# Kernel tuning notes

Measured on AMD Instinct MI355X. Metric: run time of the kernel, lower is better.

## Reference

```python
import jax, jax.numpy as jnp
import numpy as np

EPS = 1e-8
N = 1024          # number of points
C = 16            # channels per layer
RBF_LOW, RBF_HIGH, RBF_COUNT = 0.0, 3.5, 32


def _rand(key, shape, scale=0.1):
    return scale * jax.random.normal(key, shape, dtype=jnp.float32)


def setup_inputs() -> dict:
    key = jax.random.key(0)
    ks = jax.random.split(key, 20)
    R = RBF_COUNT
    return {
        'points':   jax.random.normal(ks[0], (N, 3), dtype=jnp.float32),
        # layer 1: 2 radial filters (0->0 and 0->1), output_dim = 1 input channel
        'l1_W1':    _rand(ks[1],  (2, R, R)),
        'l1_B1':    _rand(ks[2],  (2, R)),
        'l1_W2':    _rand(ks[3],  (2, R, 1)),
        'l1_B2':    _rand(ks[4],  (2, 1)),
        'l1_si0_w': _rand(ks[5],  (C, 1)),
        'l1_si0_b': _rand(ks[6],  (C,)),
        'l1_si1_w': _rand(ks[7],  (C, 1)),
        'l1_nl_b':  _rand(ks[8],  (C,)),
        # layer 2: 5 radial filters (0->0, 0->1, 1->0, 1->1 id, 1->1 levi-civita)
        'l2_W1':    _rand(ks[9],  (5, R, R)),
        'l2_B1':    _rand(ks[10], (5, R)),
        'l2_W2':    _rand(ks[11], (5, R, C)),
        'l2_B2':    _rand(ks[12], (5, C)),
        'l2_si0_w': _rand(ks[13], (C, 2 * C)),
        'l2_si0_b': _rand(ks[14], (C,)),
        'l2_si1_w': _rand(ks[15], (C, 3 * C)),
        'l2_nl_b':  _rand(ks[16], (C,)),
        # readout
        'fc_w':     _rand(ks[17], (C, 8)),
        'fc_b':     _rand(ks[18], (8,)),
    }


def _eijk():
    e = np.zeros((3, 3, 3), dtype=np.float32)
    e[0, 1, 2] = e[1, 2, 0] = e[2, 0, 1] = 1.0
    e[0, 2, 1] = e[2, 1, 0] = e[1, 0, 2] = -1.0
    return jnp.asarray(e)


def _norm_eps(x, axis, keepdims=False):
    # norm_with_epsilon: sqrt(max(sum(x^2), EPS))
    return jnp.sqrt(jnp.maximum(jnp.sum(x * x, axis=axis, keepdims=keepdims), EPS))


def _radial(rbf, w1, b1, w2, b2):
    # R(): two-layer relu MLP on rbf features -> [N, N, F]
    h = jax.nn.relu(rbf @ w1 + b1)
    return h @ w2 + b2


def _geometry(points):
    rij = points[:, None, :] - points[None, :, :]          # [N,N,3]
    ss = jnp.sum(rij * rij, axis=-1)                        # [N,N]
    mask0 = ss < EPS                                        # dij == 0 (diagonal)
    dij = jnp.where(mask0, 0.0, jnp.sqrt(jnp.where(mask0, 1.0, ss)))
    centers = jnp.linspace(RBF_LOW, RBF_HIGH, RBF_COUNT, dtype=jnp.float32)
    gamma = jnp.float32(RBF_COUNT / (RBF_HIGH - RBF_LOW))
    rbf = jnp.exp(-gamma * (dij[..., None] - centers) ** 2)  # [N,N,RBF]
    unit = rij / _norm_eps(rij, axis=-1, keepdims=True)       # unit_vectors
    return rbf, unit, mask0


def _F1(rad, unit, mask0):
    # F_1: mask radial where dij==0, multiply by unit vectors -> [N,N,F,3]
    mr = jnp.where(mask0[..., None], 0.0, rad)
    return mr[..., None] * unit[:, :, None, :]


def _nonlinearity(x0, x1, b1):
    # degree-0: pointwise elu; degree-1: norm nonlinearity x * elu(|x|+b)/|x|
    x0 = jax.nn.elu(x0)
    n = _norm_eps(x1, axis=-1)                              # [N,C]
    x1 = x1 * (jax.nn.elu(n + b1) / n)[..., None]
    return x0, x1


def reference(points, l1_W1, l1_B1, l1_W2, l1_B2, l1_si0_w, l1_si0_b, l1_si1_w,
              l1_nl_b, l2_W1, l2_B1, l2_W2, l2_B2, l2_si0_w, l2_si0_b, l2_si1_w,
              l2_nl_b, fc_w, fc_b):
    rbf, unit, mask0 = _geometry(points)
    eijk = _eijk().astype(points.dtype)
    n_pts = points.shape[0]
    x0 = jnp.ones((n_pts, 1, 1), dtype=points.dtype)        # degree-0 input [N,1,1]

    # ---- layer 1: only degree-0 input -> (0->0) and (0->1) filters ----
    r00 = _radial(rbf, l1_W1[0], l1_B1[0], l1_W2[0], l1_B2[0])
    out0 = jnp.einsum('abf,bfi->afi', r00, x0)              # filter_0
    F1a = _F1(_radial(rbf, l1_W1[1], l1_B1[1], l1_W2[1], l1_B2[1]), unit, mask0)
    out1 = jnp.einsum('abfi,bf->afi', F1a, x0[..., 0])
    x0 = jnp.einsum('afi,gf->agi', out0, l1_si0_w) + l1_si0_b[:, None]
    x1 = jnp.einsum('afi,gf->agi', out1, l1_si1_w)
    x0, x1 = _nonlinearity(x0, x1, l1_nl_b)                 # [N,C,1], [N,C,3]

    # ---- layer 2: degree-0 and degree-1 inputs -> 5 filters ----
    rads = [_radial(rbf, l2_W1[i], l2_B1[i], l2_W2[i], l2_B2[i]) for i in range(5)]
    c00 = jnp.einsum('abf,bfi->afi', rads[0], x0)                          # 0x0->0
    c01 = jnp.einsum('abfi,bf->afi', _F1(rads[1], unit, mask0), x0[..., 0])  # 0x1->1
    c10 = jnp.einsum('abfj,bfj->af', _F1(rads[2], unit, mask0), x1)[..., None]  # 1x1->0
    c11 = jnp.einsum('abf,bfi->afi', rads[3], x1)                          # 1x0->1
    c11x = jnp.einsum('ijk,abfj,bfk->afi', eijk, _F1(rads[4], unit, mask0), x1)  # 1x1->1
    cat0 = jnp.concatenate([c00, c10], axis=-2)             # [N,2C,1]
    cat1 = jnp.concatenate([c01, c11, c11x], axis=-2)       # [N,3C,3]
    x0 = jnp.einsum('afi,gf->agi', cat0, l2_si0_w) + l2_si0_b[:, None]
    x1 = jnp.einsum('afi,gf->agi', cat1, l2_si1_w)
    x0, x1 = _nonlinearity(x0, x1, l2_nl_b)

    # ---- readout: invariant degree-0 features, mean-pool over points ----
    g = jnp.mean(x0[..., 0], axis=0)                        # [C]
    return g @ fc_w + fc_b                                  # [num_classes]
```

## Files before the change

### kernel.cpp

```cpp
#include <hip/hip_runtime.h>
#include <hip/hip_bf16.h>
#include <math.h>

#define NP 1024
#define R 32
#define C 16
#define GAMMA (32.0f/3.5f)
#define DC (3.5f/31.0f)
#define NBANK 32

typedef __attribute__((ext_vector_type(8))) short bf16x8;
typedef __attribute__((ext_vector_type(4))) float f32x4;

__device__ __forceinline__ short tobf(float x){
    __hip_bfloat16 h = __float2bfloat16(x);
    return __builtin_bit_cast(short, h);
}
__device__ __forceinline__ unsigned pack2bf(float a, float b){
    const unsigned lo = (unsigned short)tobf(a);
    const unsigned hi = (unsigned short)tobf(b);
    return lo | (hi << 16);
}
__device__ __forceinline__ float eluf(float x){ return x > 0.f ? x : expm1f(x); }

__device__ __forceinline__ f32x4 mfma16(bf16x8 a, bf16x8 b, f32x4 c){
    return __builtin_amdgcn_mfma_f32_16x16x32_bf16(a, b, c, 0, 0, 0);
}

template<int STRIDE>
__device__ __forceinline__ void load_bfrag(const float* __restrict__ src, int q, int n,
                                           bf16x8& w){
    #pragma unroll
    for (int jj = 0; jj < 8; jj++)
        w[jj] = tobf(src[(q*8+jj)*STRIDE + n]);
}

__global__ __launch_bounds__(256) void k_l1p(
    const float* __restrict__ points,
    const float* __restrict__ W1, const float* __restrict__ B1,
    const float* __restrict__ W2, const float* __restrict__ B2,
    const float* __restrict__ si0w, const float* __restrict__ si0b,
    const float* __restrict__ si1w, const float* __restrict__ nlb,
    float* __restrict__ x0g, float* __restrict__ x1s,
    float* __restrict__ c00g, float* __restrict__ c10g,
    unsigned* __restrict__ cntA,
    float* __restrict__ partial, unsigned* __restrict__ cnt)
{
    __shared__ float sS0[4][32];
    __shared__ float sT[4][32][3];
    __shared__ float sUp[4][3];
    __shared__ float sO[4];

    const int tid  = threadIdx.x;
    const int lane = tid & 63;
    const int wv   = tid >> 6;
    const int l16  = lane & 15;
    const int q    = lane >> 4;
    const int a    = blockIdx.x;
    const float pax = points[a*3+0], pay = points[a*3+1], paz = points[a*3+2];

    bf16x8 w1f[2][2];
    float  b1v[2][2];
    #pragma unroll
    for (int fi = 0; fi < 2; fi++)
        #pragma unroll
        for (int nt = 0; nt < 2; nt++){
            load_bfrag<R>(W1 + fi*R*R, q, nt*16 + l16, w1f[fi][nt]);
            b1v[fi][nt] = B1[fi*R + nt*16 + l16];
        }

    float s0a[2] = {0.f, 0.f};
    float T[2][3] = {};
    float upx = 0.f, upy = 0.f, upz = 0.f;

    for (int bt = 0; bt < 16; bt++){
        const int bA = bt*64 + wv*16 + l16;
        const float rx = pax - points[bA*3+0];
        const float ry = pay - points[bA*3+1];
        const float rz = paz - points[bA*3+2];
        const float ss = rx*rx + ry*ry + rz*rz;
        const float dij = sqrtf(ss);
        const float inv = 1.0f / sqrtf(fmaxf(ss, 1e-8f));
        const float ux = rx*inv, uy = ry*inv, uz = rz*inv;
        upx += ux; upy += uy; upz += uz;

        bf16x8 afrag;
        #pragma unroll
        for (int jj = 0; jj < 8; jj++){
            const float t = dij - (float)(q*8+jj)*DC;
            afrag[jj] = tobf(__expf(-GAMMA*t*t));
        }

        float uxr[4], uyr[4], uzr[4];
        #pragma unroll
        for (int r4 = 0; r4 < 4; r4++){
            const int sl = q*4 + r4;
            uxr[r4] = __shfl(ux, sl, 16);
            uyr[r4] = __shfl(uy, sl, 16);
            uzr[r4] = __shfl(uz, sl, 16);
        }

        #pragma unroll
        for (int nt = 0; nt < 2; nt++){
            f32x4 c = {b1v[0][nt], b1v[0][nt], b1v[0][nt], b1v[0][nt]};
            c = mfma16(afrag, w1f[0][nt], c);
            s0a[nt] += fmaxf(c[0],0.f)+fmaxf(c[1],0.f)+fmaxf(c[2],0.f)+fmaxf(c[3],0.f);
        }
        #pragma unroll
        for (int nt = 0; nt < 2; nt++){
            f32x4 c = {b1v[1][nt], b1v[1][nt], b1v[1][nt], b1v[1][nt]};
            c = mfma16(afrag, w1f[1][nt], c);
            #pragma unroll
            for (int r4 = 0; r4 < 4; r4++){
                const float h = fmaxf(c[r4], 0.f);
                T[nt][0] = fmaf(h, uxr[r4], T[nt][0]);
                T[nt][1] = fmaf(h, uyr[r4], T[nt][1]);
                T[nt][2] = fmaf(h, uzr[r4], T[nt][2]);
            }
        }
    }

    #pragma unroll
    for (int nt = 0; nt < 2; nt++){
        s0a[nt] += __shfl_down(s0a[nt], 32, 64);
        s0a[nt] += __shfl_down(s0a[nt], 16, 64);
        #pragma unroll
        for (int i = 0; i < 3; i++){
            T[nt][i] += __shfl_down(T[nt][i], 32, 64);
            T[nt][i] += __shfl_down(T[nt][i], 16, 64);
        }
    }
    #pragma unroll
    for (int off = 32; off > 0; off >>= 1){
        upx += __shfl_down(upx, off, 64);
        upy += __shfl_down(upy, off, 64);
        upz += __shfl_down(upz, off, 64);
    }
    if (lane < 16){
        sS0[wv][lane]      = s0a[0];
        sS0[wv][16 + lane] = s0a[1];
        #pragma unroll
        for (int i = 0; i < 3; i++){
            sT[wv][lane][i]      = T[0][i];
            sT[wv][16 + lane][i] = T[1][i];
        }
    }
    if (lane == 0){ sUp[wv][0] = upx; sUp[wv][1] = upy; sUp[wv][2] = upz; }
    __syncthreads();
    if (tid == 0){
        float o0 = 0.f;
        for (int j = 0; j < R; j++){
            const float S = sS0[0][j] + sS0[1][j] + sS0[2][j] + sS0[3][j];
            o0 = fmaf(S, W2[j], o0);
        }
        sO[0] = o0 + (float)NP * B2[0];
        for (int i = 0; i < 3; i++){
            float t = 0.f;
            for (int j = 0; j < R; j++){
                const float Tj = sT[0][j][i] + sT[1][j][i] + sT[2][j][i] + sT[3][j][i];
                t = fmaf(Tj, W2[R + j], t);
            }
            const float Ui = 0.25f * (sUp[0][i] + sUp[1][i] + sUp[2][i] + sUp[3][i]);
            sO[1+i] = t + B2[1] * Ui;
        }
    }
    __syncthreads();
    if (tid < C){
        const int g = tid;
        const float o0 = sO[0];
        const float o1x = sO[1], o1y = sO[2], o1z = sO[3];
        x0g[a*C+g] = eluf(fmaf(o0, si0w[g], si0b[g]));
        const float w = si1w[g];
        const float tx = o1x*w, ty = o1y*w, tz = o1z*w;
        const float n = sqrtf(fmaxf(tx*tx + ty*ty + tz*tz, 1e-8f));
        const float sc = eluf(n + nlb[g]) / n;
        x1s[0*NP*C + a*C+g] = tx*sc;
        x1s[1*NP*C + a*C+g] = ty*sc;
        x1s[2*NP*C + a*C+g] = tz*sc;
    }
    if (tid < C){ c00g[a*C + tid] = 0.f; c10g[a*C + tid] = 0.f; }
    if (tid == 0) cntA[a] = 0u;
    if (a == 0){
        partial[tid]       = 0.f;
        partial[256 + tid] = 0.f;
        if (tid < NBANK) cnt[tid] = 0u;
        if (tid == 0) cnt[NBANK] = 0u;
    }
}

__global__ __launch_bounds__(256) void k_l2r(
    const float* __restrict__ points,
    const float* __restrict__ W1, const float* __restrict__ B1,
    const float* __restrict__ W2, const float* __restrict__ B2,
    const float* __restrict__ x0g, const float* __restrict__ x1s,
    const float* __restrict__ si0w, const float* __restrict__ si0b,
    const float* __restrict__ fcw, const float* __restrict__ fcb,
    float* __restrict__ c00g, float* __restrict__ c10g,
    unsigned* __restrict__ cntA,
    float* __restrict__ partial, unsigned* __restrict__ cnt,
    float* __restrict__ out)
{
    __shared__ __align__(16) short sH[4][2][16*40];
    __shared__ float sRed[4][2][16];
    __shared__ float sP[16];
    __shared__ unsigned aDone, amLast;

    const int tid  = threadIdx.x;
    const int lane = tid & 63;
    const int wv   = tid >> 6;
    const int l16  = lane & 15;
    const int q    = lane >> 4;
    const int a    = blockIdx.x >> 1;
    const int half = blockIdx.x & 1;
    const float pax = points[a*3+0], pay = points[a*3+1], paz = points[a*3+2];

    bf16x8 w1f[2][2], w2f[2];
    float  b1v[2][2], b2v[2];
    #pragma unroll
    for (int fi = 0; fi < 2; fi++){
        const int fx = (fi == 0) ? 0 : 2;
        #pragma unroll
        for (int nt = 0; nt < 2; nt++){
            load_bfrag<R>(W1 + fx*R*R, q, 2*l16 + nt, w1f[fi][nt]);
            b1v[fi][nt] = B1[fx*R + 2*l16 + nt];
        }
        load_bfrag<C>(W2 + fx*R*C, q, l16, w2f[fi]);
        b2v[fi] = B2[fx*C + l16];
    }

    float acc0 = 0.f, acc1 = 0.f;
    short* sH0 = sH[wv][0];
    short* sH1 = sH[wv][1];

    for (int bt = half*8; bt < half*8 + 8; bt++){
        const int bA = bt*64 + wv*16 + l16;
        const float rx = pax - points[bA*3+0];
        const float ry = pay - points[bA*3+1];
        const float rz = paz - points[bA*3+2];
        const float ss = rx*rx + ry*ry + rz*rz;
        const float dij = sqrtf(ss);
        const float inv = 1.0f / sqrtf(fmaxf(ss, 1e-8f));
        const float ux = rx*inv, uy = ry*inv, uz = rz*inv;

        float uxr[4], uyr[4], uzr[4];
        #pragma unroll
        for (int r4 = 0; r4 < 4; r4++){
            const int sl = q*4 + r4;
            uxr[r4] = __shfl(ux, sl, 16);
            uyr[r4] = __shfl(uy, sl, 16);
            uzr[r4] = __shfl(uz, sl, 16);
        }

        const int rb = (bt*64 + wv*16 + q*4)*C + l16;
        float x0v[4], udv[4];
        #pragma unroll
        for (int r4 = 0; r4 < 4; r4++){
            x0v[r4] = x0g[rb + r4*C];
            const float v0 = x1s[0*NP*C + rb + r4*C];
            const float v1 = x1s[1*NP*C + rb + r4*C];
            const float v2 = x1s[2*NP*C + rb + r4*C];
            udv[r4] = uxr[r4]*v0 + uyr[r4]*v1 + uzr[r4]*v2;
        }

        bf16x8 afrag;
        #pragma unroll
        for (int jj = 0; jj < 8; jj++){
            const float t = dij - (float)(q*8+jj)*DC;
            afrag[jj] = tobf(__expf(-GAMMA*t*t));
        }

        #pragma unroll
        for (int fi = 0; fi < 2; fi++){
            f32x4 c0 = {b1v[fi][0], b1v[fi][0], b1v[fi][0], b1v[fi][0]};
            c0 = mfma16(afrag, w1f[fi][0], c0);
            f32x4 c1 = {b1v[fi][1], b1v[fi][1], b1v[fi][1], b1v[fi][1]};
            c1 = mfma16(afrag, w1f[fi][1], c1);
            short* sHf = (fi == 0) ? sH0 : sH1;
            #pragma unroll
            for (int r4 = 0; r4 < 4; r4++){
                const unsigned p = pack2bf(fmaxf(c0[r4], 0.f), fmaxf(c1[r4], 0.f));
                *(unsigned*)&sHf[(q*4+r4)*40 + 2*l16] = p;
            }
        }
        asm volatile("s_waitcnt lgkmcnt(0)" ::: "memory");

        {
            const bf16x8 hf = *(const bf16x8*)(sH0 + l16*40 + q*8);
            f32x4 d = {0.f, 0.f, 0.f, 0.f};
            d = mfma16(hf, w2f[0], d);
            #pragma unroll
            for (int r4 = 0; r4 < 4; r4++)
                acc0 = fmaf(d[r4] + b2v[0], x0v[r4], acc0);
        }
        {
            const bf16x8 hf = *(const bf16x8*)(sH1 + l16*40 + q*8);
            f32x4 d = {0.f, 0.f, 0.f, 0.f};
            d = mfma16(hf, w2f[1], d);
            #pragma unroll
            for (int r4 = 0; r4 < 4; r4++)
                acc1 = fmaf(d[r4] + b2v[1], udv[r4], acc1);
        }
    }

    acc0 += __shfl_down(acc0, 32, 64); acc0 += __shfl_down(acc0, 16, 64);
    acc1 += __shfl_down(acc1, 32, 64); acc1 += __shfl_down(acc1, 16, 64);
    if (lane < 16){ sRed[wv][0][lane] = acc0; sRed[wv][1][lane] = acc1; }
    __syncthreads();
    if (tid < 16)
        atomicAdd(&c00g[a*C + tid],
                  sRed[0][0][tid] + sRed[1][0][tid] + sRed[2][0][tid] + sRed[3][0][tid]);
    else if (tid < 32){
        const int f = tid - 16;
        atomicAdd(&c10g[a*C + f],
                  sRed[0][1][f] + sRed[1][1][f] + sRed[2][1][f] + sRed[3][1][f]);
    }
    __syncthreads();
    if (tid == 0)
        aDone = (atomicAdd(&cntA[a], 1u) == 1u) ? 1u : 0u;
    __syncthreads();

    if (aDone){
        if (tid < C){
            const int g = tid;
            float s = si0b[g];
            #pragma unroll
            for (int f = 0; f < C; f++){
                const float v0 = __hip_atomic_load(&c00g[a*C + f], __ATOMIC_RELAXED,
                                                   __HIP_MEMORY_SCOPE_AGENT);
                s = fmaf(v0, si0w[g*2*C + f], s);
            }
            #pragma unroll
            for (int f = 0; f < C; f++){
                const float v1 = __hip_atomic_load(&c10g[a*C + f], __ATOMIC_RELAXED,
                                                   __HIP_MEMORY_SCOPE_AGENT);
                s = fmaf(v1, si0w[g*2*C + C + f], s);
            }
            atomicAdd(&partial[(a & (NBANK-1))*C + g], eluf(s));
        }
        __syncthreads();
        if (tid == 0){
            amLast = 0u;
            const unsigned p1 = atomicAdd(&cnt[a & (NBANK-1)], 1u);
            if (p1 == (NP/NBANK) - 1u){
                const unsigned p2 = atomicAdd(&cnt[NBANK], 1u);
                if (p2 == NBANK - 1u) amLast = 1u;
            }
        }
        __syncthreads();
        if (amLast){
            if (tid < C){
                float v = 0.f;
                #pragma unroll
                for (int b = 0; b < NBANK; b++)
                    v += __hip_atomic_load(&partial[b*C + tid], __ATOMIC_RELAXED,
                                           __HIP_MEMORY_SCOPE_AGENT);
                sP[tid] = v;
            }
            __syncthreads();
            if (tid < 8){
                float s = fcb[tid];
                #pragma unroll
                for (int g = 0; g < C; g++)
                    s = fmaf(sP[g] * (1.0f / (float)NP), fcw[g*8 + tid], s);
                out[tid] = s;
            }
        }
    }
}

extern "C" void kernel_launch(void* const* d_in, const int* in_sizes, int n_in,
                              void* d_out, int out_size, void* d_ws, size_t ws_size,
                              hipStream_t stream)
{
    (void)in_sizes; (void)n_in; (void)out_size; (void)ws_size;
    const float* points   = (const float*)d_in[0];
    const float* l1_W1    = (const float*)d_in[1];
    const float* l1_B1    = (const float*)d_in[2];
    const float* l1_W2    = (const float*)d_in[3];
    const float* l1_B2    = (const float*)d_in[4];
    const float* l1_si0_w = (const float*)d_in[5];
    const float* l1_si0_b = (const float*)d_in[6];
    const float* l1_si1_w = (const float*)d_in[7];
    const float* l1_nl_b  = (const float*)d_in[8];
    const float* l2_W1    = (const float*)d_in[9];
    const float* l2_B1    = (const float*)d_in[10];
    const float* l2_W2    = (const float*)d_in[11];
    const float* l2_B2    = (const float*)d_in[12];
    const float* l2_si0_w = (const float*)d_in[13];
    const float* l2_si0_b = (const float*)d_in[14];
    const float* fc_w     = (const float*)d_in[17];
    const float* fc_b     = (const float*)d_in[18];

    float* ws       = (float*)d_ws;
    float* x0g      = ws;
    float* x1s      = x0g + NP*C;
    float* c00g     = x1s + 3*NP*C;
    float* c10g     = c00g + NP*C;
    float* partial  = c10g + NP*C;
    unsigned* cnt   = (unsigned*)(partial + NBANK*C);
    unsigned* cntA  = cnt + NBANK + 1;

    k_l1p<<<NP, 256, 0, stream>>>(points, l1_W1, l1_B1, l1_W2, l1_B2,
                                  l1_si0_w, l1_si0_b, l1_si1_w, l1_nl_b,
                                  x0g, x1s, c00g, c10g, cntA, partial, cnt);
    k_l2r<<<2*NP, 256, 0, stream>>>(points, l2_W1, l2_B1, l2_W2, l2_B2,
                                    x0g, x1s, l2_si0_w, l2_si0_b,
                                    fc_w, fc_b, c00g, c10g, cntA,
                                    partial, cnt, (float*)d_out);
}
```

Baseline: 155.8 us.

## Split layer-1 pass across two blocks per point with atomic merge and interleaved layout

Layer 1 now launches two blocks per point, each handling half of the neighbour tiles. W2 is applied before the reduction so only seven scalars per wave are reduced and atomically accumulated. The last-arriving block applies the nonlinearity and writes x0 and x1 interleaved as one float4 per channel, so layer 2 can load them with a single vector read. Workspace zeroing moves to a memset, which adds an extra launch plus atomic and counter overhead in exchange for more parallelism in layer 1.

```diff
diff --git a/kernel.cpp b/kernel.cpp
--- a/kernel.cpp
+++ b/kernel.cpp
@@ -41,26 +41,24 @@
     const float* __restrict__ W2, const float* __restrict__ B2,
     const float* __restrict__ si0w, const float* __restrict__ si0b,
     const float* __restrict__ si1w, const float* __restrict__ nlb,
-    float* __restrict__ x0g, float* __restrict__ x1s,
-    float* __restrict__ c00g, float* __restrict__ c10g,
-    unsigned* __restrict__ cntA,
-    float* __restrict__ partial, unsigned* __restrict__ cnt)
+    float* __restrict__ xall, float* __restrict__ l1c,
+    unsigned* __restrict__ cntL1)
 {
-    __shared__ float sS0[4][32];
-    __shared__ float sT[4][32][3];
-    __shared__ float sUp[4][3];
-    __shared__ float sO[4];
+    __shared__ float sW[4][8];
+    __shared__ float sFin[8];
+    __shared__ unsigned sAm;
 
     const int tid  = threadIdx.x;
     const int lane = tid & 63;
     const int wv   = tid >> 6;
     const int l16  = lane & 15;
     const int q    = lane >> 4;
-    const int a    = blockIdx.x;
+    const int a    = blockIdx.x >> 1;
+    const int half = blockIdx.x & 1;
     const float pax = points[a*3+0], pay = points[a*3+1], paz = points[a*3+2];
 
     bf16x8 w1f[2][2];
-    float  b1v[2][2];
+    float  b1v[2][2], w2s[2], w2t[2];
     #pragma unroll
     for (int fi = 0; fi < 2; fi++)
         #pragma unroll
@@ -68,12 +66,17 @@
             load_bfrag<R>(W1 + fi*R*R, q, nt*16 + l16, w1f[fi][nt]);
             b1v[fi][nt] = B1[fi*R + nt*16 + l16];
         }
+    #pragma unroll
+    for (int nt = 0; nt < 2; nt++){
+        w2s[nt] = W2[nt*16 + l16];
+        w2t[nt] = W2[R + nt*16 + l16];
+    }
 
     float s0a[2] = {0.f, 0.f};
     float T[2][3] = {};
     float upx = 0.f, upy = 0.f, upz = 0.f;
 
-    for (int bt = 0; bt < 16; bt++){
+    for (int bt = half*8; bt < half*8 + 8; bt++){
         const int bA = bt*64 + wv*16 + l16;
         const float rx = pax - points[bA*3+0];
         const float ry = pay - points[bA*3+1];
@@ -120,71 +123,46 @@
         }
     }
 
-    #pragma unroll
-    for (int nt = 0; nt < 2; nt++){
-        s0a[nt] += __shfl_down(s0a[nt], 32, 64);
-        s0a[nt] += __shfl_down(s0a[nt], 16, 64);
-        #pragma unroll
-        for (int i = 0; i < 3; i++){
-            T[nt][i] += __shfl_down(T[nt][i], 32, 64);
-            T[nt][i] += __shfl_down(T[nt][i], 16, 64);
-        }
-    }
-    #pragma unroll
-    for (int off = 32; off > 0; off >>= 1){
-        upx += __shfl_down(upx, off, 64);
-        upy += __shfl_down(upy, off, 64);
-        upz += __shfl_down(upz, off, 64);
-    }
-    if (lane < 16){
-        sS0[wv][lane]      = s0a[0];
-        sS0[wv][16 + lane] = s0a[1];
-        #pragma unroll
-        for (int i = 0; i < 3; i++){
-            sT[wv][lane][i]      = T[0][i];
-            sT[wv][16 + lane][i] = T[1][i];
-        }
-    }
-    if (lane == 0){ sUp[wv][0] = upx; sUp[wv][1] = upy; sUp[wv][2] = upz; }
-    __syncthreads();
-    if (tid == 0){
-        float o0 = 0.f;
-        for (int j = 0; j < R; j++){
-            const float S = sS0[0][j] + sS0[1][j] + sS0[2][j] + sS0[3][j];
-            o0 = fmaf(S, W2[j], o0);
-        }
-        sO[0] = o0 + (float)NP * B2[0];
-        for (int i = 0; i < 3; i++){
-            float t = 0.f;
-            for (int j = 0; j < R; j++){
-                const float Tj = sT[0][j][i] + sT[1][j][i] + sT[2][j][i] + sT[3][j][i];
-                t = fmaf(Tj, W2[R + j], t);
-            }
-            const float Ui = 0.25f * (sUp[0][i] + sUp[1][i] + sUp[2][i] + sUp[3][i]);
-            sO[1+i] = t + B2[1] * Ui;
-        }
-    }
-    __syncthreads();
-    if (tid < C){
-        const int g = tid;
-        const float o0 = sO[0];
-        const float o1x = sO[1], o1y = sO[2], o1z = sO[3];
-        x0g[a*C+g] = eluf(fmaf(o0, si0w[g], si0b[g]));
-        const float w = si1w[g];
-        const float tx = o1x*w, ty = o1y*w, tz = o1z*w;
-        const float n = sqrtf(fmaxf(tx*tx + ty*ty + tz*tz, 1e-8f));
-        const float sc = eluf(n + nlb[g]) / n;
-        x1s[0*NP*C + a*C+g] = tx*sc;
-        x1s[1*NP*C + a*C+g] = ty*sc;
-        x1s[2*NP*C + a*C+g] = tz*sc;
-    }
-    if (tid < C){ c00g[a*C + tid] = 0.f; c10g[a*C + tid] = 0.f; }
-    if (tid == 0) cntA[a] = 0u;
-    if (a == 0){
-        partial[tid]       = 0.f;
-        partial[256 + tid] = 0.f;
-        if (tid < NBANK) cnt[tid] = 0u;
-        if (tid == 0) cnt[NBANK] = 0u;
+    float v[7];
+    v[0] = s0a[0]*w2s[0] + s0a[1]*w2s[1];
+    #pragma unroll
+    for (int i = 0; i < 3; i++)
+        v[1+i] = T[0][i]*w2t[0] + T[1][i]*w2t[1];
+    v[4] = upx; v[5] = upy; v[6] = upz;
+    #pragma unroll
+    for (int off = 32; off > 0; off >>= 1)
+        #pragma unroll
+        for (int k = 0; k < 7; k++)
+            v[k] += __shfl_down(v[k], off, 64);
+    if (lane == 0)
+        #pragma unroll
+        for (int k = 0; k < 7; k++) sW[wv][k] = v[k];
+    __syncthreads();
+    if (tid < 7)
+        atomicAdd(&l1c[a*8 + tid], sW[0][tid] + sW[1][tid] + sW[2][tid] + sW[3][tid]);
+    __syncthreads();
+    if (tid == 0)
+        sAm = (atomicAdd(&cntL1[a], 1u) == 1u) ? 1u : 0u;
+    __syncthreads();
+    if (sAm){
+        if (tid < 7)
+            sFin[tid] = __hip_atomic_load(&l1c[a*8 + tid], __ATOMIC_RELAXED,
+                                          __HIP_MEMORY_SCOPE_AGENT);
+        __syncthreads();
+        if (tid < C){
+            const int g = tid;
+            const float o0  = sFin[0] + (float)NP * B2[0];
+            const float o1x = sFin[1] + B2[1] * 0.25f * sFin[4];
+            const float o1y = sFin[2] + B2[1] * 0.25f * sFin[5];
+            const float o1z = sFin[3] + B2[1] * 0.25f * sFin[6];
+            const float x0 = eluf(fmaf(o0, si0w[g], si0b[g]));
+            const float w = si1w[g];
+            const float tx = o1x*w, ty = o1y*w, tz = o1z*w;
+            const float n = sqrtf(fmaxf(tx*tx + ty*ty + tz*tz, 1e-8f));
+            const float sc = eluf(n + nlb[g]) / n;
+            f32x4 st = {x0, tx*sc, ty*sc, tz*sc};
+            *(f32x4*)&xall[(a*C + g)*4] = st;
+        }
     }
 }
 
@@ -192,7 +170,7 @@
     const float* __restrict__ points,
     const float* __restrict__ W1, const float* __restrict__ B1,
     const float* __restrict__ W2, const float* __restrict__ B2,
-    const float* __restrict__ x0g, const float* __restrict__ x1s,
+    const float* __restrict__ xall,
     const float* __restrict__ si0w, const float* __restrict__ si0b,
     const float* __restrict__ fcw, const float* __restrict__ fcb,
     float* __restrict__ c00g, float* __restrict__ c10g,
@@ -251,15 +229,13 @@
             uzr[r4] = __shfl(uz, sl, 16);
         }
 
-        const int rb = (bt*64 + wv*16 + q*4)*C + l16;
+        const f32x4* xp = (const f32x4*)&xall[((bt*64 + wv*16 + q*4)*C + l16)*4];
         float x0v[4], udv[4];
         #pragma unroll
         for (int r4 = 0; r4 < 4; r4++){
-            x0v[r4] = x0g[rb + r4*C];
-            const float v0 = x1s[0*NP*C + rb + r4*C];
-            const float v1 = x1s[1*NP*C + rb + r4*C];
-            const float v2 = x1s[2*NP*C + rb + r4*C];
-            udv[r4] = uxr[r4]*v0 + uyr[r4]*v1 + uzr[r4]*v2;
+            const f32x4 xv = xp[r4*C];
+            x0v[r4] = xv[0];
+            udv[r4] = uxr[r4]*xv[1] + uyr[r4]*xv[2] + uzr[r4]*xv[3];
         }
 
         bf16x8 afrag;
@@ -391,20 +367,23 @@
     const float* fc_w     = (const float*)d_in[17];
     const float* fc_b     = (const float*)d_in[18];
 
-    float* ws       = (float*)d_ws;
-    float* x0g      = ws;
-    float* x1s      = x0g + NP*C;
-    float* c00g     = x1s + 3*NP*C;
-    float* c10g     = c00g + NP*C;
-    float* partial  = c10g + NP*C;
-    unsigned* cnt   = (unsigned*)(partial + NBANK*C);
-    unsigned* cntA  = cnt + NBANK + 1;
-
-    k_l1p<<<NP, 256, 0, stream>>>(points, l1_W1, l1_B1, l1_W2, l1_B2,
-                                  l1_si0_w, l1_si0_b, l1_si1_w, l1_nl_b,
-                                  x0g, x1s, c00g, c10g, cntA, partial, cnt);
+    float* ws        = (float*)d_ws;
+    float* partial   = ws;
+    unsigned* cnt    = (unsigned*)(partial + NBANK*C);
+    unsigned* cntA   = cnt + 64;
+    unsigned* cntL1  = cntA + NP;
+    float* l1c       = (float*)(cntL1 + NP);
+    float* c00g      = l1c + NP*8;
+    float* c10g      = c00g + NP*C;
+    float* xall      = c10g + NP*C;
+    const size_t zeroBytes = (size_t)((char*)xall - (char*)ws);
+
+    hipMemsetAsync(ws, 0, zeroBytes, stream);
+    k_l1p<<<2*NP, 256, 0, stream>>>(points, l1_W1, l1_B1, l1_W2, l1_B2,
+                                    l1_si0_w, l1_si0_b, l1_si1_w, l1_nl_b,
+                                    xall, l1c, cntL1);
     k_l2r<<<2*NP, 256, 0, stream>>>(points, l2_W1, l2_B1, l2_W2, l2_B2,
-                                    x0g, x1s, l2_si0_w, l2_si0_b,
+                                    xall, l2_si0_w, l2_si0_b,
                                     fc_w, fc_b, c00g, c10g, cntA,
                                     partial, cnt, (float*)d_out);
 }
```

Result: faster. 148.9 us (-4.4%).
